# Performance work log

Hardware: AMD Instinct MI355X
Metric: run time of the kernel (lower is better)

## Reference

```python
import jax, jax.numpy as jnp
import numpy as np
import math

# ---------- real Wigner 3j (Clebsch-Gordan in real spherical-harmonic basis) ----------

def _w3j_complex(l1, l2, l3):
    F = math.factorial
    tri = F(l1 + l2 - l3) * F(l1 - l2 + l3) * F(-l1 + l2 + l3) / F(l1 + l2 + l3 + 1)
    C = np.zeros((2 * l1 + 1, 2 * l2 + 1, 2 * l3 + 1))
    for m1 in range(-l1, l1 + 1):
        for m2 in range(-l2, l2 + 1):
            m3 = -m1 - m2
            if abs(m3) > l3:
                continue
            pref = (-1.0) ** (l1 - l2 - m3) * math.sqrt(
                tri * F(l1 + m1) * F(l1 - m1) * F(l2 + m2) * F(l2 - m2) * F(l3 + m3) * F(l3 - m3))
            s = 0.0
            for t in range(max(0, l2 - l3 - m1, l1 - l3 + m2),
                           min(l1 + l2 - l3, l1 - m1, l2 + m2) + 1):
                s += (-1.0) ** t / (F(t) * F(l1 + l2 - l3 - t) * F(l1 - m1 - t)
                                    * F(l2 + m2 - t) * F(l3 - l2 + m1 + t) * F(l3 - l1 - m2 + t))
            C[m1 + l1, m2 + l2, m3 + l3] = pref * s
    return C

def _U_real(l):
    # complex -> real spherical harmonic change of basis, rows indexed by real m in [-l, l]
    U = np.zeros((2 * l + 1, 2 * l + 1), dtype=complex)
    U[l, l] = 1.0
    s2 = 1.0 / math.sqrt(2.0)
    for m in range(1, l + 1):
        U[l + m, l + m] = (-1) ** m * s2
        U[l + m, l - m] = s2
        U[l - m, l - m] = 1j * s2
        U[l - m, l + m] = -1j * (-1) ** m * s2
    return U

def _w3j_real(l1, l2, l3):
    # 3j symbol is rotation invariant, so conjugating each index by U gives the real-basis 3j;
    # for even l1+l2+l3 (all paths here) the result is purely real. Frobenius norm is 1.
    Cc = _w3j_complex(l1, l2, l3)
    Cr = np.einsum('ia,jb,kc,abc->ijk', _U_real(l1), _U_real(l2), _U_real(l3), Cc)
    return np.ascontiguousarray(Cr.real.astype(np.float32))

_PATHS = [(4, 4), (4, 6), (6, 4), (6, 6)]  # CG-allowed couplings into 4e and into 6e
_CG = {(l1, l2, lo): jnp.asarray(_w3j_real(l1, l2, lo)) for lo in (4, 6) for (l1, l2) in _PATHS}
_A4 = math.sqrt(9.0 / 4.0)    # component normalization: sqrt(dim(4e) / n_paths)
_A6 = math.sqrt(13.0 / 4.0)   # component normalization: sqrt(dim(6e) / n_paths)
_K = 3                        # kernel_size
_COPIES = 4                   # upsample_factor**2


def setup_inputs() -> dict:
    key = jax.random.key(0)
    k1, k2, k3 = jax.random.split(key, 3)
    H = W = 768
    n = H * W
    return {
        'f4': jax.random.normal(k1, (n, 9), dtype=jnp.float32),
        'f6': jax.random.normal(k2, (n, 13), dtype=jnp.float32),
        'spatial_weights': jnp.ones((_K, _K), dtype=jnp.float32) / (_K * _K),
        'tp_weights': jax.random.normal(k3, (_COPIES, 8), dtype=jnp.float32),
        'H': H, 'W': W,
    }


def reference(f4, f6, spatial_weights, tp_weights, H, W):
    feats = jnp.concatenate([f4, f6], axis=-1)            # (HW, 22)
    Cch = feats.shape[-1]
    img = feats.reshape(H, W, Cch)
    pad = _K // 2
    img_p = jnp.pad(img, ((pad, pad), (pad, pad), (0, 0)), mode='edge')  # replicate padding
    # weighted 3x3 neighbor sum == depthwise conv with the shared spatial kernel
    kern = jnp.broadcast_to(spatial_weights[:, :, None, None], (_K, _K, 1, Cch)).astype(feats.dtype)
    nb = jax.lax.conv_general_dilated(
        img_p[None], kern, (1, 1), 'VALID',
        dimension_numbers=('NHWC', 'HWIO', 'NHWC'),
        feature_group_count=Cch)[0].reshape(-1, Cch)      # (HW, 22)

    x = {4: feats[:, :9], 6: feats[:, 9:]}                # center-pixel irreps
    y = {4: nb[:, :9], 6: nb[:, 9:]}                      # neighbor-aggregated irreps
    # path outputs are shared across copies; only the scalar path weights differ per copy
    t4 = jnp.stack([jnp.einsum('ijk,ni,nj->nk', _CG[(l1, l2, 4)], x[l1], y[l2]) for l1, l2 in _PATHS], 0)  # (4, HW, 9)
    t6 = jnp.stack([jnp.einsum('ijk,ni,nj->nk', _CG[(l1, l2, 6)], x[l1], y[l2]) for l1, l2 in _PATHS], 0)  # (4, HW, 13)
    out4 = _A4 * jnp.einsum('cp,pnk->nck', tp_weights[:, :4], t4)   # (HW, copies, 9)
    out6 = _A6 * jnp.einsum('cp,pnk->nck', tp_weights[:, 4:], t6)   # (HW, copies, 13)
    # per-copy [f4(9) | f6(13)] blocks concatenated along features, as in torch.cat(out_per_copy, -1)
    out = jnp.concatenate([out4, out6], axis=-1).reshape(-1, _COPIES * 22)  # (HW, 88)
    f4_size = 9 * _COPIES
    f4_out = out[:, :f4_size] + jnp.tile(f4, (1, _COPIES))   # matches torch's :36 slice + repeat residual
    f6_out = out[:, f4_size:] + jnp.tile(f6, (1, _COPIES))
    return f4_out, f6_out
```

## Files before the change

### kernel.cpp

```cpp
#include <hip/hip_runtime.h>
#include <utility>
#include <cstddef>
#include <cmath>

namespace cg {

struct FactTab { double f[24]; };
constexpr FactTab make_fact() {
  FactTab t{}; t.f[0] = 1.0;
  for (int i = 1; i < 24; ++i) t.f[i] = t.f[i-1] * (double)i;
  return t;
}
constexpr FactTab FT = make_fact();
constexpr double F(int n) { return FT.f[n]; }

constexpr double csqrt(double x) {
  if (x <= 0.0) return 0.0;
  double g = x > 1.0 ? x : 1.0;
  for (int i = 0; i < 200; ++i) {
    double ng = 0.5 * (g + x / g);
    if (ng >= g) break;
    g = ng;
  }
  return g;
}

struct T3 { double v[13][13][13]; };

constexpr T3 w3j_c(int l1, int l2, int l3) {
  T3 C{};
  const double tri = F(l1+l2-l3) * F(l1-l2+l3) * F(-l1+l2+l3) / F(l1+l2+l3+1);
  for (int m1 = -l1; m1 <= l1; ++m1) {
    for (int m2 = -l2; m2 <= l2; ++m2) {
      const int m3 = -m1 - m2;
      if (m3 < -l3 || m3 > l3) continue;
      const int e = l1 - l2 - m3;
      const double sign = (((e % 2) + 2) % 2) ? -1.0 : 1.0;
      const double pref = sign * csqrt(tri * F(l1+m1) * F(l1-m1) * F(l2+m2)
                                           * F(l2-m2) * F(l3+m3) * F(l3-m3));
      int t0 = 0;
      if (l2 - l3 - m1 > t0) t0 = l2 - l3 - m1;
      if (l1 - l3 + m2 > t0) t0 = l1 - l3 + m2;
      int t1 = l1 + l2 - l3;
      if (l1 - m1 < t1) t1 = l1 - m1;
      if (l2 + m2 < t1) t1 = l2 + m2;
      double s = 0.0;
      for (int t = t0; t <= t1; ++t) {
        const double term = 1.0 / (F(t) * F(l1+l2-l3-t) * F(l1-m1-t)
                                   * F(l2+m2-t) * F(l3-l2+m1+t) * F(l3-l1-m2+t));
        s += (t % 2) ? -term : term;
      }
      C.v[m1+l1][m2+l2][m3+l3] = pref * s;
    }
  }
  return C;
}

struct C2 { double re, im; };
constexpr C2 cmul(C2 a, C2 b) { return C2{a.re*b.re - a.im*b.im, a.re*b.im + a.im*b.re}; }

struct UCol { int n; int row[2]; C2 val[2]; };
constexpr UCol ucol(int l, int a) {
  UCol r{};
  const double s2 = csqrt(0.5);
  if (a == l) {
    r.n = 1; r.row[0] = l; r.val[0] = C2{1.0, 0.0};
  } else if (a > l) {
    const int m = a - l;
    const double sg = (m % 2) ? -1.0 : 1.0;
    r.n = 2;
    r.row[0] = l + m; r.val[0] = C2{sg * s2, 0.0};
    r.row[1] = l - m; r.val[1] = C2{0.0, -sg * s2};
  } else {
    const int m = l - a;
    r.n = 2;
    r.row[0] = l + m; r.val[0] = C2{s2, 0.0};
    r.row[1] = l - m; r.val[1] = C2{0.0, s2};
  }
  return r;
}

constexpr T3 to_real(const T3& Cc, int l1, int l2, int l3) {
  T3 R{};
  UCol U1[13]{}, U2[13]{}, U3[13]{};
  for (int a = 0; a < 2*l1+1; ++a) U1[a] = ucol(l1, a);
  for (int b = 0; b < 2*l2+1; ++b) U2[b] = ucol(l2, b);
  for (int c = 0; c < 2*l3+1; ++c) U3[c] = ucol(l3, c);
  for (int a = 0; a < 2*l1+1; ++a)
    for (int b = 0; b < 2*l2+1; ++b)
      for (int c = 0; c < 2*l3+1; ++c) {
        const double cv = Cc.v[a][b][c];
        if (cv == 0.0) continue;
        for (int ia = 0; ia < U1[a].n; ++ia)
          for (int jb = 0; jb < U2[b].n; ++jb)
            for (int kc = 0; kc < U3[c].n; ++kc) {
              C2 t = cmul(cmul(U1[a].val[ia], U2[b].val[jb]), U3[c].val[kc]);
              R.v[U1[a].row[ia]][U2[b].row[jb]][U3[c].row[kc]] += t.re * cv;
            }
      }
  return R;
}

struct Ent { short i, j, k; float v; };
constexpr int CAP = 1100;
template <int C> struct List { int n; Ent e[C]; };

constexpr List<CAP> make_list(const T3& R, int d1, int d2, int d3) {
  List<CAP> L{};
  for (int i = 0; i < d1; ++i)
    for (int j = 0; j < d2; ++j)
      for (int k = 0; k < d3; ++k) {
        const double v = R.v[i][j][k];
        if (v > 1e-10 || v < -1e-10) {
          L.e[L.n].i = (short)i; L.e[L.n].j = (short)j; L.e[L.n].k = (short)k;
          L.e[L.n].v = (float)v;
          L.n++;
        }
      }
  return L;
}

constexpr T3 CC444 = w3j_c(4,4,4);
constexpr T3 CC446 = w3j_c(4,4,6);
constexpr T3 CC464 = w3j_c(4,6,4);
constexpr T3 CC466 = w3j_c(4,6,6);
constexpr T3 CC644 = w3j_c(6,4,4);
constexpr T3 CC646 = w3j_c(6,4,6);
constexpr T3 CC664 = w3j_c(6,6,4);
constexpr T3 CC666 = w3j_c(6,6,6);

constexpr T3 CR444 = to_real(CC444, 4,4,4);
constexpr T3 CR446 = to_real(CC446, 4,4,6);
constexpr T3 CR464 = to_real(CC464, 4,6,4);
constexpr T3 CR466 = to_real(CC466, 4,6,6);
constexpr T3 CR644 = to_real(CC644, 6,4,4);
constexpr T3 CR646 = to_real(CC646, 6,4,6);
constexpr T3 CR664 = to_real(CC664, 6,6,4);
constexpr T3 CR666 = to_real(CC666, 6,6,6);

struct Tag444 { static constexpr List<CAP> L = make_list(CR444, 9, 9, 9);  };
struct Tag446 { static constexpr List<CAP> L = make_list(CR446, 9, 9, 13); };
struct Tag464 { static constexpr List<CAP> L = make_list(CR464, 9, 13, 9); };
struct Tag466 { static constexpr List<CAP> L = make_list(CR466, 9, 13, 13);};
struct Tag644 { static constexpr List<CAP> L = make_list(CR644, 13, 9, 9); };
struct Tag646 { static constexpr List<CAP> L = make_list(CR646, 13, 9, 13);};
struct Tag664 { static constexpr List<CAP> L = make_list(CR664, 13, 13, 9);};
struct Tag666 { static constexpr List<CAP> L = make_list(CR666, 13, 13, 13);};

template <class Tag, size_t... Es>
__device__ __forceinline__ void cg_apply_impl(const float* __restrict__ x,
                                              const float* __restrict__ y,
                                              float* __restrict__ acc,
                                              std::index_sequence<Es...>) {
  ((acc[(int)Tag::L.e[Es].k] +=
        Tag::L.e[Es].v * (x[(int)Tag::L.e[Es].i] * y[(int)Tag::L.e[Es].j])), ...);
}
template <class Tag>
__device__ __forceinline__ void cg_apply(const float* __restrict__ x,
                                         const float* __restrict__ y,
                                         float* __restrict__ acc) {
  cg_apply_impl<Tag>(x, y, acc, std::make_index_sequence<(size_t)Tag::L.n>{});
}

}

__global__ __launch_bounds__(256) void conv_kernel(
    const float* __restrict__ f4, const float* __restrict__ f6,
    const float* __restrict__ sw,
    const int* __restrict__ Hp, const int* __restrict__ Wp,
    float* __restrict__ nb4, float* __restrict__ nb6) {
  const int H = Hp[0], W = Wp[0];
  const int n = H * W;
  const int n9 = n * 9;
  const int total = n * 22;
  const int idx = blockIdx.x * 256 + threadIdx.x;
  if (idx >= total) return;

  float w[9];
#pragma unroll
  for (int t = 0; t < 9; ++t) w[t] = sw[t];

  if (idx < n9) {
    const int p = idx / 9, ch = idx - 9 * p;
    const int py = p / W, px = p - py * W;
    float acc = 0.0f;
#pragma unroll
    for (int dy = -1; dy <= 1; ++dy) {
      int yy = py + dy; yy = yy < 0 ? 0 : (yy >= H ? H - 1 : yy);
#pragma unroll
      for (int dx = -1; dx <= 1; ++dx) {
        int xx = px + dx; xx = xx < 0 ? 0 : (xx >= W ? W - 1 : xx);
        acc += w[(dy + 1) * 3 + (dx + 1)] * f4[(size_t)(yy * W + xx) * 9 + ch];
      }
    }
    nb4[idx] = acc;
  } else {
    const int j = idx - n9;
    const int p = j / 13, ch = j - 13 * p;
    const int py = p / W, px = p - py * W;
    float acc = 0.0f;
#pragma unroll
    for (int dy = -1; dy <= 1; ++dy) {
      int yy = py + dy; yy = yy < 0 ? 0 : (yy >= H ? H - 1 : yy);
#pragma unroll
      for (int dx = -1; dx <= 1; ++dx) {
        int xx = px + dx; xx = xx < 0 ? 0 : (xx >= W ? W - 1 : xx);
        acc += w[(dy + 1) * 3 + (dx + 1)] * f6[(size_t)(yy * W + xx) * 13 + ch];
      }
    }
    nb6[j] = acc;
  }
}

__global__ __launch_bounds__(256) void cgc_kernel(
    const float* __restrict__ f4, const float* __restrict__ f6,
    const float* __restrict__ nb4, const float* __restrict__ nb6,
    const float* __restrict__ tpw,
    const int* __restrict__ Hp, const int* __restrict__ Wp,
    float* __restrict__ out) {
  const int H = Hp[0], W = Wp[0];
  const int n = H * W;
  const int p = blockIdx.x * 256 + threadIdx.x;
  if (p >= n) return;

  float x4[9], x6[13], y4[9], y6[13];
  {
    const float* a = f4 + (size_t)p * 9;
#pragma unroll
    for (int c = 0; c < 9; ++c) x4[c] = a[c];
    const float* b = f6 + (size_t)p * 13;
#pragma unroll
    for (int c = 0; c < 13; ++c) x6[c] = b[c];
    const float* cy = nb4 + (size_t)p * 9;
#pragma unroll
    for (int c = 0; c < 9; ++c) y4[c] = cy[c];
    const float* d = nb6 + (size_t)p * 13;
#pragma unroll
    for (int c = 0; c < 13; ++c) y6[c] = d[c];
  }

  float t4[4][9];
  float t6[4][13];
#pragma unroll
  for (int pth = 0; pth < 4; ++pth) {
#pragma unroll
    for (int k = 0; k < 9; ++k) t4[pth][k] = 0.0f;
#pragma unroll
    for (int k = 0; k < 13; ++k) t6[pth][k] = 0.0f;
  }

  cg::cg_apply<cg::Tag444>(x4, y4, t4[0]);
  cg::cg_apply<cg::Tag446>(x4, y4, t6[0]);
  cg::cg_apply<cg::Tag464>(x4, y6, t4[1]);
  cg::cg_apply<cg::Tag466>(x4, y6, t6[1]);
  cg::cg_apply<cg::Tag644>(x6, y4, t4[2]);
  cg::cg_apply<cg::Tag646>(x6, y4, t6[2]);
  cg::cg_apply<cg::Tag664>(x6, y6, t4[3]);
  cg::cg_apply<cg::Tag666>(x6, y6, t6[3]);

  const float A4 = 1.5f;
  const float A6 = 1.8027756377319946f;

  float o4r[36];
  float o6r[52];
#pragma unroll
  for (int c = 0; c < 4; ++c) {
    const float w40 = tpw[c * 8 + 0], w41 = tpw[c * 8 + 1];
    const float w42 = tpw[c * 8 + 2], w43 = tpw[c * 8 + 3];
    const float w60 = tpw[c * 8 + 4], w61 = tpw[c * 8 + 5];
    const float w62 = tpw[c * 8 + 6], w63 = tpw[c * 8 + 7];
#pragma unroll
    for (int k = 0; k < 9; ++k) {
      const float v = A4 * (w40 * t4[0][k] + w41 * t4[1][k] +
                            w42 * t4[2][k] + w43 * t4[3][k]);
      const int flat = c * 22 + k;
      if (flat < 36) o4r[flat] = v;
      else           o6r[flat - 36] = v;
    }
#pragma unroll
    for (int k = 0; k < 13; ++k) {
      const float v = A6 * (w60 * t6[0][k] + w61 * t6[1][k] +
                            w62 * t6[2][k] + w63 * t6[3][k]);
      const int flat = c * 22 + 9 + k;
      if (flat < 36) o4r[flat] = v;
      else           o6r[flat - 36] = v;
    }
  }
#pragma unroll
  for (int j = 0; j < 36; ++j) o4r[j] += x4[j % 9];
#pragma unroll
  for (int j = 0; j < 52; ++j) o6r[j] += x6[j % 13];

  float* __restrict__ o4p = out + (size_t)p * 36;
  float* __restrict__ o6p = out + (size_t)n * 36 + (size_t)p * 52;
#pragma unroll
  for (int q = 0; q < 9; ++q) {
    float4 v; v.x = o4r[4*q+0]; v.y = o4r[4*q+1]; v.z = o4r[4*q+2]; v.w = o4r[4*q+3];
    reinterpret_cast<float4*>(o4p)[q] = v;
  }
#pragma unroll
  for (int q = 0; q < 13; ++q) {
    float4 v; v.x = o6r[4*q+0]; v.y = o6r[4*q+1]; v.z = o6r[4*q+2]; v.w = o6r[4*q+3];
    reinterpret_cast<float4*>(o6p)[q] = v;
  }
}

__global__ __launch_bounds__(256) void fused_kernel(
    const float* __restrict__ f4, const float* __restrict__ f6,
    const float* __restrict__ sw, const float* __restrict__ tpw,
    const int* __restrict__ Hp, const int* __restrict__ Wp,
    float* __restrict__ out) {
  const int H = Hp[0], W = Wp[0];
  const int n = H * W;
  const int p = blockIdx.x * 256 + threadIdx.x;
  if (p >= n) return;
  const int py = p / W;
  const int px = p - py * W;

  float x4[9], x6[13];
  {
    const float* b4 = f4 + (size_t)p * 9;
#pragma unroll
    for (int c = 0; c < 9; ++c) x4[c] = b4[c];
    const float* b6 = f6 + (size_t)p * 13;
#pragma unroll
    for (int c = 0; c < 13; ++c) x6[c] = b6[c];
  }
  float w[9];
#pragma unroll
  for (int t = 0; t < 9; ++t) w[t] = sw[t];

  float y4[9], y6[13];
#pragma unroll
  for (int c = 0; c < 9; ++c) y4[c] = w[4] * x4[c];
#pragma unroll
  for (int c = 0; c < 13; ++c) y6[c] = w[4] * x6[c];
#pragma unroll
  for (int dy = -1; dy <= 1; ++dy) {
#pragma unroll
    for (int dx = -1; dx <= 1; ++dx) {
      if (dy == 0 && dx == 0) continue;
      int yy = py + dy; yy = yy < 0 ? 0 : (yy >= H ? H - 1 : yy);
      int xx = px + dx; xx = xx < 0 ? 0 : (xx >= W ? W - 1 : xx);
      const int q = yy * W + xx;
      const float wt = w[(dy + 1) * 3 + (dx + 1)];
      const float* b4 = f4 + (size_t)q * 9;
#pragma unroll
      for (int c = 0; c < 9; ++c) y4[c] += wt * b4[c];
      const float* b6 = f6 + (size_t)q * 13;
#pragma unroll
      for (int c = 0; c < 13; ++c) y6[c] += wt * b6[c];
    }
  }

  float t4[4][9];
  float t6[4][13];
#pragma unroll
  for (int pth = 0; pth < 4; ++pth) {
#pragma unroll
    for (int k = 0; k < 9; ++k) t4[pth][k] = 0.0f;
#pragma unroll
    for (int k = 0; k < 13; ++k) t6[pth][k] = 0.0f;
  }
  cg::cg_apply<cg::Tag444>(x4, y4, t4[0]);
  cg::cg_apply<cg::Tag446>(x4, y4, t6[0]);
  cg::cg_apply<cg::Tag464>(x4, y6, t4[1]);
  cg::cg_apply<cg::Tag466>(x4, y6, t6[1]);
  cg::cg_apply<cg::Tag644>(x6, y4, t4[2]);
  cg::cg_apply<cg::Tag646>(x6, y4, t6[2]);
  cg::cg_apply<cg::Tag664>(x6, y6, t4[3]);
  cg::cg_apply<cg::Tag666>(x6, y6, t6[3]);

  const float A4 = 1.5f;
  const float A6 = 1.8027756377319946f;
  float o4r[36];
  float o6r[52];
#pragma unroll
  for (int c = 0; c < 4; ++c) {
    const float w40 = tpw[c * 8 + 0], w41 = tpw[c * 8 + 1];
    const float w42 = tpw[c * 8 + 2], w43 = tpw[c * 8 + 3];
    const float w60 = tpw[c * 8 + 4], w61 = tpw[c * 8 + 5];
    const float w62 = tpw[c * 8 + 6], w63 = tpw[c * 8 + 7];
#pragma unroll
    for (int k = 0; k < 9; ++k) {
      const float v = A4 * (w40 * t4[0][k] + w41 * t4[1][k] +
                            w42 * t4[2][k] + w43 * t4[3][k]);
      const int flat = c * 22 + k;
      if (flat < 36) o4r[flat] = v;
      else           o6r[flat - 36] = v;
    }
#pragma unroll
    for (int k = 0; k < 13; ++k) {
      const float v = A6 * (w60 * t6[0][k] + w61 * t6[1][k] +
                            w62 * t6[2][k] + w63 * t6[3][k]);
      const int flat = c * 22 + 9 + k;
      if (flat < 36) o4r[flat] = v;
      else           o6r[flat - 36] = v;
    }
  }
#pragma unroll
  for (int j = 0; j < 36; ++j) o4r[j] += x4[j % 9];
#pragma unroll
  for (int j = 0; j < 52; ++j) o6r[j] += x6[j % 13];

  float* __restrict__ o4p = out + (size_t)p * 36;
  float* __restrict__ o6p = out + (size_t)n * 36 + (size_t)p * 52;
#pragma unroll
  for (int q = 0; q < 9; ++q) {
    float4 v; v.x = o4r[4*q+0]; v.y = o4r[4*q+1]; v.z = o4r[4*q+2]; v.w = o4r[4*q+3];
    reinterpret_cast<float4*>(o4p)[q] = v;
  }
#pragma unroll
  for (int q = 0; q < 13; ++q) {
    float4 v; v.x = o6r[4*q+0]; v.y = o6r[4*q+1]; v.z = o6r[4*q+2]; v.w = o6r[4*q+3];
    reinterpret_cast<float4*>(o6p)[q] = v;
  }
}

extern "C" void kernel_launch(void* const* d_in, const int* in_sizes, int n_in,
                              void* d_out, int out_size, void* d_ws, size_t ws_size,
                              hipStream_t stream) {
  const float* f4  = (const float*)d_in[0];
  const float* f6  = (const float*)d_in[1];
  const float* sw  = (const float*)d_in[2];
  const float* tpw = (const float*)d_in[3];
  const int*   Hp  = (const int*)d_in[4];
  const int*   Wp  = (const int*)d_in[5];
  float* out = (float*)d_out;

  const int n = in_sizes[0] / 9;
  const size_t need = (size_t)n * 22 * sizeof(float);

  if (ws_size >= need) {
    float* nb4 = (float*)d_ws;
    float* nb6 = nb4 + (size_t)n * 9;
    const int convBlocks = (n * 22 + 255) / 256;
    conv_kernel<<<dim3(convBlocks), dim3(256), 0, stream>>>(
        f4, f6, sw, Hp, Wp, nb4, nb6);
    const int cgBlocks = (n + 255) / 256;
    cgc_kernel<<<dim3(cgBlocks), dim3(256), 0, stream>>>(
        f4, f6, nb4, nb6, tpw, Hp, Wp, out);
  } else {
    const int blocks = (n + 255) / 256;
    fused_kernel<<<dim3(blocks), dim3(256), 0, stream>>>(
        f4, f6, sw, tpw, Hp, Wp, out);
  }
}
```

Before: 373.0 us.

## Vectorize depthwise conv and split CG kernel into l=4/l=6 thread roles

```diff
diff --git a/kernel.cpp b/kernel.cpp
--- a/kernel.cpp
+++ b/kernel.cpp
@@ -164,6 +164,9 @@
 
 }
 
+typedef float v4u __attribute__((ext_vector_type(4), aligned(4)));
+typedef float v4a __attribute__((ext_vector_type(4), aligned(16)));
+
 __global__ __launch_bounds__(256) void conv_kernel(
     const float* __restrict__ f4, const float* __restrict__ f6,
     const float* __restrict__ sw,
@@ -171,48 +174,65 @@
     float* __restrict__ nb4, float* __restrict__ nb6) {
   const int H = Hp[0], W = Wp[0];
   const int n = H * W;
-  const int n9 = n * 9;
-  const int total = n * 22;
-  const int idx = blockIdx.x * 256 + threadIdx.x;
-  if (idx >= total) return;
+  const int g4 = (n * 9 + 3) / 4;
+  const int g6 = (n * 13 + 3) / 4;
+  const int t = blockIdx.x * 256 + threadIdx.x;
+  if (t >= g4 + g6) return;
 
   float w[9];
 #pragma unroll
-  for (int t = 0; t < 9; ++t) w[t] = sw[t];
-
-  if (idx < n9) {
-    const int p = idx / 9, ch = idx - 9 * p;
-    const int py = p / W, px = p - py * W;
-    float acc = 0.0f;
+  for (int q = 0; q < 9; ++q) w[q] = sw[q];
+
+  const bool is6 = (t >= g4);
+  const int C = is6 ? 13 : 9;
+  const float* __restrict__ src = is6 ? f6 : f4;
+  float* __restrict__ dst = is6 ? nb6 : nb4;
+  const int base = (is6 ? (t - g4) : t) * 4;
+  const int total = n * C;
+
+  const int p0 = base / C;
+  const int p1 = (base + 3) / C;
+  const int py0 = p0 / W, px0 = p0 - py0 * W;
+  const int py1 = p1 / W, px1 = p1 - py1 * W;
+
+  const bool fast = (base + 3 < total) &&
+                    (px0 >= 1) && (py0 >= 1) && (px1 <= W - 2) && (py1 <= H - 2);
+
+  if (fast) {
+    v4u acc = {0.f, 0.f, 0.f, 0.f};
 #pragma unroll
     for (int dy = -1; dy <= 1; ++dy) {
-      int yy = py + dy; yy = yy < 0 ? 0 : (yy >= H ? H - 1 : yy);
 #pragma unroll
       for (int dx = -1; dx <= 1; ++dx) {
-        int xx = px + dx; xx = xx < 0 ? 0 : (xx >= W ? W - 1 : xx);
-        acc += w[(dy + 1) * 3 + (dx + 1)] * f4[(size_t)(yy * W + xx) * 9 + ch];
-      }
-    }
-    nb4[idx] = acc;
+        const int off = (dy * W + dx) * C;
+        const v4u v = *reinterpret_cast<const v4u*>(src + base + off);
+        acc += w[(dy + 1) * 3 + (dx + 1)] * v;
+      }
+    }
+    *reinterpret_cast<v4a*>(dst + base) = (v4a)acc;
   } else {
-    const int j = idx - n9;
-    const int p = j / 13, ch = j - 13 * p;
-    const int py = p / W, px = p - py * W;
-    float acc = 0.0f;
-#pragma unroll
-    for (int dy = -1; dy <= 1; ++dy) {
-      int yy = py + dy; yy = yy < 0 ? 0 : (yy >= H ? H - 1 : yy);
-#pragma unroll
-      for (int dx = -1; dx <= 1; ++dx) {
-        int xx = px + dx; xx = xx < 0 ? 0 : (xx >= W ? W - 1 : xx);
-        acc += w[(dy + 1) * 3 + (dx + 1)] * f6[(size_t)(yy * W + xx) * 13 + ch];
-      }
-    }
-    nb6[j] = acc;
-  }
-}
-
-__global__ __launch_bounds__(256) void cgc_kernel(
+#pragma unroll
+    for (int q = 0; q < 4; ++q) {
+      const int wd = base + q;
+      if (wd >= total) break;
+      const int p = wd / C, ch = wd - C * p;
+      const int py = p / W, px = p - py * W;
+      float acc = 0.0f;
+#pragma unroll
+      for (int dy = -1; dy <= 1; ++dy) {
+        int yy = py + dy; yy = yy < 0 ? 0 : (yy >= H ? H - 1 : yy);
+#pragma unroll
+        for (int dx = -1; dx <= 1; ++dx) {
+          int xx = px + dx; xx = xx < 0 ? 0 : (xx >= W ? W - 1 : xx);
+          acc += w[(dy + 1) * 3 + (dx + 1)] * src[(size_t)(yy * W + xx) * C + ch];
+        }
+      }
+      dst[wd] = acc;
+    }
+  }
+}
+
+__global__ __launch_bounds__(256, 4) void cgc_kernel(
     const float* __restrict__ f4, const float* __restrict__ f6,
     const float* __restrict__ nb4, const float* __restrict__ nb6,
     const float* __restrict__ tpw,
@@ -220,88 +240,88 @@
     float* __restrict__ out) {
   const int H = Hp[0], W = Wp[0];
   const int n = H * W;
-  const int p = blockIdx.x * 256 + threadIdx.x;
+  const int tid = threadIdx.x;
+  const bool role6 = tid >= 128;
+  const int p = blockIdx.x * 128 + (tid & 127);
   if (p >= n) return;
 
   float x4[9], x6[13], y4[9], y6[13];
   {
     const float* a = f4 + (size_t)p * 9;
-#pragma unroll
-    for (int c = 0; c < 9; ++c) x4[c] = a[c];
+    v4u v0 = *reinterpret_cast<const v4u*>(a);
+    v4u v1 = *reinterpret_cast<const v4u*>(a + 4);
+#pragma unroll
+    for (int c = 0; c < 4; ++c) { x4[c] = v0[c]; x4[c+4] = v1[c]; }
+    x4[8] = a[8];
     const float* b = f6 + (size_t)p * 13;
-#pragma unroll
-    for (int c = 0; c < 13; ++c) x6[c] = b[c];
-    const float* cy = nb4 + (size_t)p * 9;
-#pragma unroll
-    for (int c = 0; c < 9; ++c) y4[c] = cy[c];
+    v4u u0 = *reinterpret_cast<const v4u*>(b);
+    v4u u1 = *reinterpret_cast<const v4u*>(b + 4);
+    v4u u2 = *reinterpret_cast<const v4u*>(b + 8);
+#pragma unroll
+    for (int c = 0; c < 4; ++c) { x6[c] = u0[c]; x6[c+4] = u1[c]; x6[c+8] = u2[c]; }
+    x6[12] = b[12];
+    const float* cc = nb4 + (size_t)p * 9;
+    v4u w0 = *reinterpret_cast<const v4u*>(cc);
+    v4u w1 = *reinterpret_cast<const v4u*>(cc + 4);
+#pragma unroll
+    for (int c = 0; c < 4; ++c) { y4[c] = w0[c]; y4[c+4] = w1[c]; }
+    y4[8] = cc[8];
     const float* d = nb6 + (size_t)p * 13;
-#pragma unroll
-    for (int c = 0; c < 13; ++c) y6[c] = d[c];
-  }
-
-  float t4[4][9];
-  float t6[4][13];
-#pragma unroll
-  for (int pth = 0; pth < 4; ++pth) {
-#pragma unroll
-    for (int k = 0; k < 9; ++k) t4[pth][k] = 0.0f;
-#pragma unroll
-    for (int k = 0; k < 13; ++k) t6[pth][k] = 0.0f;
-  }
-
-  cg::cg_apply<cg::Tag444>(x4, y4, t4[0]);
-  cg::cg_apply<cg::Tag446>(x4, y4, t6[0]);
-  cg::cg_apply<cg::Tag464>(x4, y6, t4[1]);
-  cg::cg_apply<cg::Tag466>(x4, y6, t6[1]);
-  cg::cg_apply<cg::Tag644>(x6, y4, t4[2]);
-  cg::cg_apply<cg::Tag646>(x6, y4, t6[2]);
-  cg::cg_apply<cg::Tag664>(x6, y6, t4[3]);
-  cg::cg_apply<cg::Tag666>(x6, y6, t6[3]);
-
-  const float A4 = 1.5f;
-  const float A6 = 1.8027756377319946f;
-
-  float o4r[36];
-  float o6r[52];
-#pragma unroll
-  for (int c = 0; c < 4; ++c) {
-    const float w40 = tpw[c * 8 + 0], w41 = tpw[c * 8 + 1];
-    const float w42 = tpw[c * 8 + 2], w43 = tpw[c * 8 + 3];
-    const float w60 = tpw[c * 8 + 4], w61 = tpw[c * 8 + 5];
-    const float w62 = tpw[c * 8 + 6], w63 = tpw[c * 8 + 7];
-#pragma unroll
-    for (int k = 0; k < 9; ++k) {
-      const float v = A4 * (w40 * t4[0][k] + w41 * t4[1][k] +
-                            w42 * t4[2][k] + w43 * t4[3][k]);
-      const int flat = c * 22 + k;
-      if (flat < 36) o4r[flat] = v;
-      else           o6r[flat - 36] = v;
-    }
-#pragma unroll
-    for (int k = 0; k < 13; ++k) {
-      const float v = A6 * (w60 * t6[0][k] + w61 * t6[1][k] +
-                            w62 * t6[2][k] + w63 * t6[3][k]);
-      const int flat = c * 22 + 9 + k;
-      if (flat < 36) o4r[flat] = v;
-      else           o6r[flat - 36] = v;
-    }
-  }
-#pragma unroll
-  for (int j = 0; j < 36; ++j) o4r[j] += x4[j % 9];
-#pragma unroll
-  for (int j = 0; j < 52; ++j) o6r[j] += x6[j % 13];
+    v4u z0 = *reinterpret_cast<const v4u*>(d);
+    v4u z1 = *reinterpret_cast<const v4u*>(d + 4);
+    v4u z2 = *reinterpret_cast<const v4u*>(d + 8);
+#pragma unroll
+    for (int c = 0; c < 4; ++c) { y6[c] = z0[c]; y6[c+4] = z1[c]; y6[c+8] = z2[c]; }
+    y6[12] = d[12];
+  }
 
   float* __restrict__ o4p = out + (size_t)p * 36;
   float* __restrict__ o6p = out + (size_t)n * 36 + (size_t)p * 52;
-#pragma unroll
-  for (int q = 0; q < 9; ++q) {
-    float4 v; v.x = o4r[4*q+0]; v.y = o4r[4*q+1]; v.z = o4r[4*q+2]; v.w = o4r[4*q+3];
-    reinterpret_cast<float4*>(o4p)[q] = v;
-  }
-#pragma unroll
-  for (int q = 0; q < 13; ++q) {
-    float4 v; v.x = o6r[4*q+0]; v.y = o6r[4*q+1]; v.z = o6r[4*q+2]; v.w = o6r[4*q+3];
-    reinterpret_cast<float4*>(o6p)[q] = v;
+
+  if (!role6) {
+    float t0[9], t1[9], t2[9], t3[9];
+#pragma unroll
+    for (int k = 0; k < 9; ++k) { t0[k] = t1[k] = t2[k] = t3[k] = 0.0f; }
+    cg::cg_apply<cg::Tag444>(x4, y4, t0);
+    cg::cg_apply<cg::Tag464>(x4, y6, t1);
+    cg::cg_apply<cg::Tag644>(x6, y4, t2);
+    cg::cg_apply<cg::Tag664>(x6, y6, t3);
+
+    const float A4 = 1.5f;
+#pragma unroll
+    for (int c = 0; c < 4; ++c) {
+      const float w0 = tpw[c * 8 + 0], w1 = tpw[c * 8 + 1];
+      const float w2 = tpw[c * 8 + 2], w3 = tpw[c * 8 + 3];
+#pragma unroll
+      for (int k = 0; k < 9; ++k) {
+        const int flat = c * 22 + k;
+        float v = A4 * (w0 * t0[k] + w1 * t1[k] + w2 * t2[k] + w3 * t3[k]);
+        if (flat < 36) { v += x4[flat % 9];        o4p[flat] = v; }
+        else           { v += x6[(flat - 36) % 13]; o6p[flat - 36] = v; }
+      }
+    }
+  } else {
+    float s0[13], s1[13], s2[13], s3[13];
+#pragma unroll
+    for (int k = 0; k < 13; ++k) { s0[k] = s1[k] = s2[k] = s3[k] = 0.0f; }
+    cg::cg_apply<cg::Tag446>(x4, y4, s0);
+    cg::cg_apply<cg::Tag466>(x4, y6, s1);
+    cg::cg_apply<cg::Tag646>(x6, y4, s2);
+    cg::cg_apply<cg::Tag666>(x6, y6, s3);
+
+    const float A6 = 1.8027756377319946f;
+#pragma unroll
+    for (int c = 0; c < 4; ++c) {
+      const float w0 = tpw[c * 8 + 4], w1 = tpw[c * 8 + 5];
+      const float w2 = tpw[c * 8 + 6], w3 = tpw[c * 8 + 7];
+#pragma unroll
+      for (int k = 0; k < 13; ++k) {
+        const int flat = c * 22 + 9 + k;
+        float v = A6 * (w0 * s0[k] + w1 * s1[k] + w2 * s2[k] + w3 * s3[k]);
+        if (flat < 36) { v += x4[flat % 9];        o4p[flat] = v; }
+        else           { v += x6[(flat - 36) % 13]; o6p[flat - 36] = v; }
+      }
+    }
   }
 }
 
@@ -373,8 +393,8 @@
 
   const float A4 = 1.5f;
   const float A6 = 1.8027756377319946f;
-  float o4r[36];
-  float o6r[52];
+  float* __restrict__ o4p = out + (size_t)p * 36;
+  float* __restrict__ o6p = out + (size_t)n * 36 + (size_t)p * 52;
 #pragma unroll
   for (int c = 0; c < 4; ++c) {
     const float w40 = tpw[c * 8 + 0], w41 = tpw[c * 8 + 1];
@@ -383,37 +403,20 @@
     const float w62 = tpw[c * 8 + 6], w63 = tpw[c * 8 + 7];
 #pragma unroll
     for (int k = 0; k < 9; ++k) {
-      const float v = A4 * (w40 * t4[0][k] + w41 * t4[1][k] +
-                            w42 * t4[2][k] + w43 * t4[3][k]);
+      float v = A4 * (w40 * t4[0][k] + w41 * t4[1][k] +
+                      w42 * t4[2][k] + w43 * t4[3][k]);
       const int flat = c * 22 + k;
-      if (flat < 36) o4r[flat] = v;
-      else           o6r[flat - 36] = v;
+      if (flat < 36) { v += x4[flat % 9];        o4p[flat] = v; }
+      else           { v += x6[(flat - 36) % 13]; o6p[flat - 36] = v; }
     }
 #pragma unroll
     for (int k = 0; k < 13; ++k) {
-      const float v = A6 * (w60 * t6[0][k] + w61 * t6[1][k] +
-                            w62 * t6[2][k] + w63 * t6[3][k]);
+      float v = A6 * (w60 * t6[0][k] + w61 * t6[1][k] +
+                      w62 * t6[2][k] + w63 * t6[3][k]);
       const int flat = c * 22 + 9 + k;
-      if (flat < 36) o4r[flat] = v;
-      else           o6r[flat - 36] = v;
-    }
-  }
-#pragma unroll
-  for (int j = 0; j < 36; ++j) o4r[j] += x4[j % 9];
-#pragma unroll
-  for (int j = 0; j < 52; ++j) o6r[j] += x6[j % 13];
-
-  float* __restrict__ o4p = out + (size_t)p * 36;
-  float* __restrict__ o6p = out + (size_t)n * 36 + (size_t)p * 52;
-#pragma unroll
-  for (int q = 0; q < 9; ++q) {
-    float4 v; v.x = o4r[4*q+0]; v.y = o4r[4*q+1]; v.z = o4r[4*q+2]; v.w = o4r[4*q+3];
-    reinterpret_cast<float4*>(o4p)[q] = v;
-  }
-#pragma unroll
-  for (int q = 0; q < 13; ++q) {
-    float4 v; v.x = o6r[4*q+0]; v.y = o6r[4*q+1]; v.z = o6r[4*q+2]; v.w = o6r[4*q+3];
-    reinterpret_cast<float4*>(o6p)[q] = v;
+      if (flat < 36) { v += x4[flat % 9];        o4p[flat] = v; }
+      else           { v += x6[(flat - 36) % 13]; o6p[flat - 36] = v; }
+    }
   }
 }
 
@@ -434,10 +437,12 @@
   if (ws_size >= need) {
     float* nb4 = (float*)d_ws;
     float* nb6 = nb4 + (size_t)n * 9;
-    const int convBlocks = (n * 22 + 255) / 256;
+    const int g4 = (n * 9 + 3) / 4;
+    const int g6 = (n * 13 + 3) / 4;
+    const int convBlocks = (g4 + g6 + 255) / 256;
     conv_kernel<<<dim3(convBlocks), dim3(256), 0, stream>>>(
         f4, f6, sw, Hp, Wp, nb4, nb6);
-    const int cgBlocks = (n + 255) / 256;
+    const int cgBlocks = (n + 127) / 128;
     cgc_kernel<<<dim3(cgBlocks), dim3(256), 0, stream>>>(
         f4, f6, nb4, nb6, tpw, Hp, Wp, out);
   } else {
```

After: 811.5 us. +117.6%, slower.
